# Kernel optimization log

Hardware: AMD Instinct MI355X
Metric: run time of the kernel (lower is better)

The kernel has to match this reference:

```python
import jax, jax.numpy as jnp
import numpy as np

STRIDE = 10  # matches init_kwargs

def setup_inputs() -> dict:
    key = jax.random.key(0)
    x = jax.random.normal(key, (64, 1000, 128), dtype=jnp.float32)
    return {"x": x}

def reference(x):
    B, T, F = x.shape
    L = T // STRIDE  # number of windows
    # (B, L, S, F): non-overlapping windows of length STRIDE
    xr = x.reshape(B, L, STRIDE, F)
    mean = xr.mean(axis=2, keepdims=True)          # avg_pool(ksize=stride, strides=stride)
    ms = xr - mean                                  # means_subtracted
    std = jnp.sqrt(jnp.mean(ms * ms, axis=2))       # (B, L, F), population std
    # per-window covariance: (B, L, F, F)
    cov = jnp.einsum('blsk,blsm->blkm', ms, ms) / STRIDE
    # strictly-lower-triangle indices, row-major order == tf.boolean_mask order
    i, j = np.tril_indices(F, -1)
    cov_v = cov[..., i, j]                          # (B, L, F*(F-1)/2)
    den_v = std[..., i] * std[..., j]               # gather std pairs directly
    safe = jnp.where(den_v == 0, jnp.float32(1.0), den_v)
    return jnp.where(den_v == 0, jnp.float32(0.0), cov_v / safe)  # divide_no_nan
```

## Files before the change

### kernel.cpp

```cpp
#include <hip/hip_runtime.h>

#define BATCH 64
#define TLEN 1000
#define F 128
#define S 10
#define L 100
#define NPAIR 8128
#define NTILE 528

__global__ __launch_bounds__(256) void corr_kernel(const float* __restrict__ x,
                                                   float* __restrict__ out) {
    const int win = blockIdx.x;
    const int b = win / L;
    const int l = win % L;
    const int tid = threadIdx.x;

    __shared__ float ms[S][F];
    __shared__ float stdv[F];

    const float* src = x + ((size_t)b * TLEN + (size_t)l * S) * F;
    const float4* src4 = (const float4*)src;
    float4* lds4 = (float4*)&ms[0][0];
    for (int i = tid; i < (S * F) / 4; i += 256) {
        lds4[i] = src4[i];
    }
    __syncthreads();

    if (tid < F) {
        const int f = tid;
        float col[S];
        float sum = 0.f;
        #pragma unroll
        for (int s = 0; s < S; ++s) { col[s] = ms[s][f]; sum += col[s]; }
        const float mean = sum / (float)S;
        float sq = 0.f;
        #pragma unroll
        for (int s = 0; s < S; ++s) { float d = col[s] - mean; col[s] = d; sq += d * d; }
        #pragma unroll
        for (int s = 0; s < S; ++s) ms[s][f] = col[s];
        stdv[f] = sqrtf(sq / (float)S);
    }
    __syncthreads();

    float* outw = out + (size_t)win * NPAIR;

    for (int t = tid; t < NTILE; t += 256) {
        int ti = (int)((sqrtf(8.0f * (float)t + 1.0f) - 1.0f) * 0.5f);
        while ((ti + 1) * (ti + 2) / 2 <= t) ++ti;
        while (ti * (ti + 1) / 2 > t) --ti;
        const int tj = t - ti * (ti + 1) / 2;

        float acc[4][4];
        #pragma unroll
        for (int a = 0; a < 4; ++a)
            #pragma unroll
            for (int c = 0; c < 4; ++c) acc[a][c] = 0.f;

        #pragma unroll
        for (int s = 0; s < S; ++s) {
            const float4 av = *(const float4*)&ms[s][ti * 4];
            const float4 bv = *(const float4*)&ms[s][tj * 4];
            const float a0[4] = {av.x, av.y, av.z, av.w};
            const float b0[4] = {bv.x, bv.y, bv.z, bv.w};
            #pragma unroll
            for (int di = 0; di < 4; ++di)
                #pragma unroll
                for (int dj = 0; dj < 4; ++dj)
                    acc[di][dj] += a0[di] * b0[dj];
        }

        float sa[4], sb[4];
        #pragma unroll
        for (int d = 0; d < 4; ++d) { sa[d] = stdv[ti * 4 + d]; sb[d] = stdv[tj * 4 + d]; }

        #pragma unroll
        for (int di = 0; di < 4; ++di) {
            const int i = ti * 4 + di;
            #pragma unroll
            for (int dj = 0; dj < 4; ++dj) {
                const int j = tj * 4 + dj;
                if (j < i) {
                    const float den = sa[di] * sb[dj];
                    const float cov = acc[di][dj] / (float)S;
                    outw[i * (i - 1) / 2 + j] = (den == 0.f) ? 0.f : cov / den;
                }
            }
        }
    }
}

extern "C" void kernel_launch(void* const* d_in, const int* in_sizes, int n_in,
                              void* d_out, int out_size, void* d_ws, size_t ws_size,
                              hipStream_t stream) {
    const float* x = (const float*)d_in[0];
    float* out = (float*)d_out;
    corr_kernel<<<BATCH * L, 256, 0, stream>>>(x, out);
}
```

Baseline: 273.8 us.

## Pre-normalize by std, stage triangle in LDS, write coalesced float4 output

Each column is scaled by 1/(sqrt(S)*std) once, so the inner products directly give correlations and the per-pair division disappears. The scattered per-element global stores are replaced by writes into an LDS buffer holding the window's triangle, followed by a coalesced float4 copy to global memory. The block size goes to 512 threads with a 32KB LDS buffer, which raises LDS use per block and may limit occupancy. Pre-scaling changes rounding slightly, and the std==0 case is handled by zeroing the normalized column.

Measured after the change: 252.4 us. 7.8% less time.

```diff
diff --git a/kernel.cpp b/kernel.cpp
--- a/kernel.cpp
+++ b/kernel.cpp
@@ -7,23 +7,21 @@
 #define L 100
 #define NPAIR 8128
 #define NTILE 528
+#define NT4 (NPAIR / 4)
+#define BLOCK 512
 
-__global__ __launch_bounds__(256) void corr_kernel(const float* __restrict__ x,
-                                                   float* __restrict__ out) {
+__global__ __launch_bounds__(BLOCK, 8) void corr_kernel(const float* __restrict__ x,
+                                                        float* __restrict__ out) {
     const int win = blockIdx.x;
     const int b = win / L;
     const int l = win % L;
     const int tid = threadIdx.x;
 
     __shared__ float ms[S][F];
-    __shared__ float stdv[F];
+    __shared__ __align__(16) float tri[NPAIR];
 
-    const float* src = x + ((size_t)b * TLEN + (size_t)l * S) * F;
-    const float4* src4 = (const float4*)src;
-    float4* lds4 = (float4*)&ms[0][0];
-    for (int i = tid; i < (S * F) / 4; i += 256) {
-        lds4[i] = src4[i];
-    }
+    const float4* src4 = (const float4*)(x + ((size_t)b * TLEN + (size_t)l * S) * F);
+    if (tid < (S * F) / 4) ((float4*)&ms[0][0])[tid] = src4[tid];
     __syncthreads();
 
     if (tid < F) {
@@ -32,19 +30,18 @@
         float sum = 0.f;
         #pragma unroll
         for (int s = 0; s < S; ++s) { col[s] = ms[s][f]; sum += col[s]; }
-        const float mean = sum / (float)S;
+        const float mean = sum * (1.0f / S);
         float sq = 0.f;
         #pragma unroll
         for (int s = 0; s < S; ++s) { float d = col[s] - mean; col[s] = d; sq += d * d; }
+        const float stdv = sqrtf(sq * (1.0f / S));
+        const float r = (stdv == 0.f) ? 0.f : 0.31622776601683794f / stdv;
         #pragma unroll
-        for (int s = 0; s < S; ++s) ms[s][f] = col[s];
-        stdv[f] = sqrtf(sq / (float)S);
+        for (int s = 0; s < S; ++s) ms[s][f] = col[s] * r;
     }
     __syncthreads();
 
-    float* outw = out + (size_t)win * NPAIR;
-
-    for (int t = tid; t < NTILE; t += 256) {
+    for (int t = tid; t < NTILE; t += BLOCK) {
         int ti = (int)((sqrtf(8.0f * (float)t + 1.0f) - 1.0f) * 0.5f);
         while ((ti + 1) * (ti + 2) / 2 <= t) ++ti;
         while (ti * (ti + 1) / 2 > t) --ti;
@@ -69,24 +66,23 @@
                     acc[di][dj] += a0[di] * b0[dj];
         }
 
-        float sa[4], sb[4];
-        #pragma unroll
-        for (int d = 0; d < 4; ++d) { sa[d] = stdv[ti * 4 + d]; sb[d] = stdv[tj * 4 + d]; }
-
         #pragma unroll
         for (int di = 0; di < 4; ++di) {
             const int i = ti * 4 + di;
+            const int rowoff = i * (i - 1) / 2 + tj * 4;
             #pragma unroll
-            for (int dj = 0; dj < 4; ++dj) {
+            for (int k = 0; k < 4; ++k) {
+                const int dj = (k + tid) & 3;
                 const int j = tj * 4 + dj;
-                if (j < i) {
-                    const float den = sa[di] * sb[dj];
-                    const float cov = acc[di][dj] / (float)S;
-                    outw[i * (i - 1) / 2 + j] = (den == 0.f) ? 0.f : cov / den;
-                }
+                if (j < i) tri[rowoff + dj] = acc[di][dj];
             }
         }
     }
+    __syncthreads();
+
+    const float4* t4 = (const float4*)tri;
+    float4* o4 = (float4*)(out + (size_t)win * NPAIR);
+    for (int p = tid; p < NT4; p += BLOCK) o4[p] = t4[p];
 }
 
 extern "C" void kernel_launch(void* const* d_in, const int* in_sizes, int n_in,
@@ -94,5 +90,5 @@
                               hipStream_t stream) {
     const float* x = (const float*)d_in[0];
     float* out = (float*)d_out;
-    corr_kernel<<<BATCH * L, 256, 0, stream>>>(x, out);
+    corr_kernel<<<BATCH * L, BLOCK, 0, stream>>>(x, out);
 }
```
